# Kernel optimization log

Hardware: AMD Instinct MI355X
Metric: run time of the kernel (lower is better)

The kernel has to match this reference:

```python
import jax, jax.numpy as jnp
import numpy as np
import math

D_MODEL = 512
N_HEADS = 8
MAX_SEQ_LEN = 4096
DENSITY = 0.3


def _make_random_mask(key, seq_len, density=DENSITY):
    # rand < density, symmetrized via (m + m.T)/2, clamped to [0,1], diag = 1
    u = jax.random.uniform(key, (seq_len, seq_len), dtype=jnp.float32)
    m = (u < density).astype(jnp.float32)
    m = jnp.clip((m + m.T) * 0.5, 0.0, 1.0)
    return m.at[jnp.diag_indices(seq_len)].set(1.0)


def setup_inputs() -> dict:
    key = jax.random.key(0)
    ks = jax.random.split(key, 10)
    B, T, C = 2, 4096, D_MODEL
    scale = 1.0 / math.sqrt(C)
    x = jax.random.normal(ks[0], (B, T, C), dtype=jnp.float32)
    mask = _make_random_mask(ks[1], MAX_SEQ_LEN)[:T, :T]
    # Linear weights stored as (in, out): y = x @ W + b
    Wq = jax.random.normal(ks[2], (C, C), dtype=jnp.float32) * scale
    Wk = jax.random.normal(ks[3], (C, C), dtype=jnp.float32) * scale
    Wv = jax.random.normal(ks[4], (C, C), dtype=jnp.float32) * scale
    Wo = jax.random.normal(ks[5], (C, C), dtype=jnp.float32) * scale
    bq = jax.random.normal(ks[6], (C,), dtype=jnp.float32) * scale
    bk = jax.random.normal(ks[7], (C,), dtype=jnp.float32) * scale
    bv = jax.random.normal(ks[8], (C,), dtype=jnp.float32) * scale
    bo = jax.random.normal(ks[9], (C,), dtype=jnp.float32) * scale
    return {"x": x, "mask": mask, "Wq": Wq, "bq": bq, "Wk": Wk, "bk": bk,
            "Wv": Wv, "bv": bv, "Wo": Wo, "bo": bo}


def reference(x, mask, Wq, bq, Wk, bk, Wv, bv, Wo, bo):
    B, T, C = x.shape
    H = N_HEADS
    dk = C // H
    q = (x @ Wq + bq).reshape(B, T, H, dk)
    k = (x @ Wk + bk).reshape(B, T, H, dk)
    v = (x @ Wv + bv).reshape(B, T, H, dk)
    # scores: [B, H, T, T]
    attn = jnp.einsum('bthd,bshd->bhts', q, k) / math.sqrt(dk)
    attn = attn * mask[None, None, :, :]  # multiplicative mask PRE-softmax
    p = jax.nn.softmax(attn, axis=-1)
    out = jnp.einsum('bhts,bshd->bthd', p, v).reshape(B, T, C)
    return out @ Wo + bo
```

## Files before the change

kernel.cpp:

```cpp
#include <hip/hip_runtime.h>
#include <math.h>

#define D_MODEL 512
#define N_HEADS 8
#define DK 64
#define QSCALE (0.0625f * 1.44269504089f)

typedef __attribute__((ext_vector_type(8))) short short8;
typedef __attribute__((ext_vector_type(4))) float f32x4;
typedef __attribute__((ext_vector_type(16))) float f32x16;

typedef __attribute__((address_space(1))) const unsigned as1_uint;
typedef __attribute__((address_space(3))) unsigned as3_uint;

__device__ __forceinline__ unsigned short f2bf(float f) {
    unsigned u = __builtin_bit_cast(unsigned, f);
    u = (u + 0x7fff + ((u >> 16) & 1)) >> 16;
    return (unsigned short)u;
}

__global__ __launch_bounds__(256) void cvt_x_kernel(const float* __restrict__ x,
                                                    unsigned short* __restrict__ xb, int n8)
{
    int i = blockIdx.x * 256 + threadIdx.x;
    if (i >= n8) return;
    float4 a = ((const float4*)x)[i * 2];
    float4 b = ((const float4*)x)[i * 2 + 1];
    short8 o;
    o[0] = f2bf(a.x); o[1] = f2bf(a.y); o[2] = f2bf(a.z); o[3] = f2bf(a.w);
    o[4] = f2bf(b.x); o[5] = f2bf(b.y); o[6] = f2bf(b.z); o[7] = f2bf(b.w);
    ((short8*)xb)[i] = o;
}

__global__ __launch_bounds__(256) void cvt_mask_kernel(const float* __restrict__ m,
                                                       unsigned char* __restrict__ mu, int n4)
{
    int i = blockIdx.x * 256 + threadIdx.x;
    if (i >= n4) return;
    float4 v = ((const float4*)m)[i];
    uchar4 o = { (unsigned char)(v.x * 2.0f + 0.5f),
                 (unsigned char)(v.y * 2.0f + 0.5f),
                 (unsigned char)(v.z * 2.0f + 0.5f),
                 (unsigned char)(v.w * 2.0f + 0.5f) };
    ((uchar4*)mu)[i] = o;
}

__global__ __launch_bounds__(256) void cvt_wt4_kernel(
    const float* __restrict__ Wq, const float* __restrict__ Wk,
    const float* __restrict__ Wv, const float* __restrict__ Wo,
    unsigned short* __restrict__ Wt)
{
    __shared__ float tile[64][65];
    int z = blockIdx.z;
    const float* W = (z == 0) ? Wq : (z == 1) ? Wk : (z == 2) ? Wv : Wo;
    unsigned short* dst = Wt + (size_t)z * D_MODEL * D_MODEL;
    int t = threadIdx.x;
    int c0 = blockIdx.x * 64;
    int r0 = blockIdx.y * 64;
    #pragma unroll
    for (int i = 0; i < 16; i++) {
        int e = i * 256 + t, r = e >> 6, c = e & 63;
        tile[c][r] = W[(size_t)(r0 + r) * D_MODEL + c0 + c];
    }
    __syncthreads();
    #pragma unroll
    for (int i = 0; i < 16; i++) {
        int e = i * 256 + t, n = e >> 6, kk = e & 63;
        dst[(size_t)(c0 + n) * D_MODEL + r0 + kk] = f2bf(tile[n][kk]);
    }
}

__global__ __launch_bounds__(512) void gemm_qkv_kernel(
    const unsigned short* __restrict__ A, const unsigned short* __restrict__ Wt,
    const float* __restrict__ bq, const float* __restrict__ bk, const float* __restrict__ bv,
    unsigned short* __restrict__ qb, unsigned short* __restrict__ kb,
    unsigned short* __restrict__ vb, int M, int T)
{
    constexpr int K = D_MODEL;
    __shared__ unsigned short As[2][128 * 32];
    __shared__ unsigned short Bs[2][128 * 32];
    int t = threadIdx.x;
    int lane = t & 63, w = t >> 6;
    int ql = lane & 15, kg = lane >> 4;
    int m0 = blockIdx.y * 128, n0 = blockIdx.x * 128;
    int wm = w >> 2, wn = w & 3;
    bool vmode = (n0 >= 1024);

    const unsigned short* srcA = A + (size_t)(m0 + (t >> 2)) * K + (t & 3) * 8;
    const unsigned short* srcB = Wt + (size_t)(n0 + (t >> 2)) * K + (t & 3) * 8;

    f32x4 acc[4][2];
    #pragma unroll
    for (int i = 0; i < 4; i++)
        #pragma unroll
        for (int j = 0; j < 2; j++) { f32x4 z = {0.f, 0.f, 0.f, 0.f}; acc[i][j] = z; }

    constexpr int NIT = K / 32;
    int cur = 0;
    __builtin_amdgcn_global_load_lds((as1_uint*)(srcA),
        (as3_uint*)((char*)&As[0][0] + w * 1024), 16, 0, 0);
    __builtin_amdgcn_global_load_lds((as1_uint*)(srcB),
        (as3_uint*)((char*)&Bs[0][0] + w * 1024), 16, 0, 0);
    __syncthreads();

    for (int it = 0; it < NIT; ++it) {
        if (it + 1 < NIT) {
            int k0 = (it + 1) * 32;
            __builtin_amdgcn_global_load_lds((as1_uint*)(srcA + k0),
                (as3_uint*)((char*)&As[cur ^ 1][0] + w * 1024), 16, 0, 0);
            __builtin_amdgcn_global_load_lds((as1_uint*)(srcB + k0),
                (as3_uint*)((char*)&Bs[cur ^ 1][0] + w * 1024), 16, 0, 0);
        }
        short8 af[4], bfr[2];
        #pragma unroll
        for (int fm = 0; fm < 4; fm++)
            af[fm] = *(const short8*)((const char*)&As[cur][0] + (wm * 64 + fm * 16 + ql) * 64 + kg * 16);
        #pragma unroll
        for (int fn = 0; fn < 2; fn++)
            bfr[fn] = *(const short8*)((const char*)&Bs[cur][0] + (wn * 32 + fn * 16 + ql) * 64 + kg * 16);
        if (vmode) {
            #pragma unroll
            for (int fm = 0; fm < 4; fm++)
                #pragma unroll
                for (int fn = 0; fn < 2; fn++)
                    acc[fm][fn] = __builtin_amdgcn_mfma_f32_16x16x32_bf16(bfr[fn], af[fm], acc[fm][fn], 0, 0, 0);
        } else {
            #pragma unroll
            for (int fm = 0; fm < 4; fm++)
                #pragma unroll
                for (int fn = 0; fn < 2; fn++)
                    acc[fm][fn] = __builtin_amdgcn_mfma_f32_16x16x32_bf16(af[fm], bfr[fn], acc[fm][fn], 0, 0, 0);
        }
        __syncthreads();
        cur ^= 1;
    }

    #pragma unroll
    for (int fm = 0; fm < 4; fm++) {
        #pragma unroll
        for (int fn = 0; fn < 2; fn++) {
            if (vmode) {
                int m = m0 + wm * 64 + fm * 16 + ql;
                int b = m / T, tt = m % T;
                #pragma unroll
                for (int r = 0; r < 4; r++) {
                    int n = (n0 - 1024) + wn * 32 + fn * 16 + kg * 4 + r;
                    float val = acc[fm][fn][r] + bv[n];
                    int h = n >> 6, d = n & 63;
                    vb[((size_t)(b * N_HEADS + h) * DK + d) * T + tt] = f2bf(val);
                }
            } else {
                int n = n0 + wn * 32 + fn * 16 + ql;
                int nn = n & 511;
                bool isq = (n0 < 512);
                float bn = isq ? bq[nn] : bk[nn];
                unsigned short* dst = isq ? qb : kb;
                int h = nn >> 6, d = nn & 63;
                #pragma unroll
                for (int r = 0; r < 4; r++) {
                    int m = m0 + wm * 64 + fm * 16 + kg * 4 + r;
                    int b = m / T, tt = m % T;
                    float val = acc[fm][fn][r] + bn;
                    if (isq) val *= QSCALE;
                    dst[((size_t)(b * N_HEADS + h) * T + tt) * DK + d] = f2bf(val);
                }
            }
        }
    }
}

__global__ __launch_bounds__(512) void gemm_out_kernel(
    const unsigned short* __restrict__ A, const unsigned short* __restrict__ Bt,
    const float* __restrict__ bias, float* __restrict__ outp, int M)
{
    constexpr int K = D_MODEL;
    __shared__ unsigned short As[2][128 * 32];
    __shared__ unsigned short Bs[2][128 * 32];
    int t = threadIdx.x;
    int lane = t & 63, w = t >> 6;
    int ql = lane & 15, kg = lane >> 4;
    int m0 = blockIdx.y * 128, n0 = blockIdx.x * 128;
    int wm = w >> 2, wn = w & 3;

    const unsigned short* srcA = A + (size_t)(m0 + (t >> 2)) * K + (t & 3) * 8;
    const unsigned short* srcB = Bt + (size_t)(n0 + (t >> 2)) * K + (t & 3) * 8;

    f32x4 acc[4][2];
    #pragma unroll
    for (int i = 0; i < 4; i++)
        #pragma unroll
        for (int j = 0; j < 2; j++) { f32x4 z = {0.f, 0.f, 0.f, 0.f}; acc[i][j] = z; }

    constexpr int NIT = K / 32;
    int cur = 0;
    __builtin_amdgcn_global_load_lds((as1_uint*)(srcA),
        (as3_uint*)((char*)&As[0][0] + w * 1024), 16, 0, 0);
    __builtin_amdgcn_global_load_lds((as1_uint*)(srcB),
        (as3_uint*)((char*)&Bs[0][0] + w * 1024), 16, 0, 0);
    __syncthreads();

    for (int it = 0; it < NIT; ++it) {
        if (it + 1 < NIT) {
            int k0 = (it + 1) * 32;
            __builtin_amdgcn_global_load_lds((as1_uint*)(srcA + k0),
                (as3_uint*)((char*)&As[cur ^ 1][0] + w * 1024), 16, 0, 0);
            __builtin_amdgcn_global_load_lds((as1_uint*)(srcB + k0),
                (as3_uint*)((char*)&Bs[cur ^ 1][0] + w * 1024), 16, 0, 0);
        }
        short8 af[4], bfr[2];
        #pragma unroll
        for (int fm = 0; fm < 4; fm++)
            af[fm] = *(const short8*)((const char*)&As[cur][0] + (wm * 64 + fm * 16 + ql) * 64 + kg * 16);
        #pragma unroll
        for (int fn = 0; fn < 2; fn++)
            bfr[fn] = *(const short8*)((const char*)&Bs[cur][0] + (wn * 32 + fn * 16 + ql) * 64 + kg * 16);
        #pragma unroll
        for (int fm = 0; fm < 4; fm++)
            #pragma unroll
            for (int fn = 0; fn < 2; fn++)
                acc[fm][fn] = __builtin_amdgcn_mfma_f32_16x16x32_bf16(af[fm], bfr[fn], acc[fm][fn], 0, 0, 0);
        __syncthreads();
        cur ^= 1;
    }

    #pragma unroll
    for (int fm = 0; fm < 4; fm++) {
        #pragma unroll
        for (int fn = 0; fn < 2; fn++) {
            int n = n0 + wn * 32 + fn * 16 + ql;
            float bn = bias[n];
            #pragma unroll
            for (int r = 0; r < 4; r++) {
                int m = m0 + wm * 64 + fm * 16 + kg * 4 + r;
                outp[(size_t)m * D_MODEL + n] = acc[fm][fn][r] + bn;
            }
        }
    }
}

__global__ __launch_bounds__(256) void attn_mfma_kernel(
    const unsigned short* __restrict__ q, const unsigned short* __restrict__ k,
    const unsigned short* __restrict__ v, const unsigned char* __restrict__ mu,
    unsigned short* __restrict__ out, int B, int T)
{
    __shared__ unsigned short Ks[2][64 * 64];
    __shared__ unsigned short Vt[2][64 * 64];

    int t = threadIdx.x;
    int lane = t & 63, w = t >> 6;
    int ln = lane & 31, hi = lane >> 5;

    int n = blockIdx.x;
    int nbh = B * N_HEADS;
    int nqt = T / 128;
    int bh, qt;
    if (nbh == 16 && nqt == 32) {
        int xcd = n & 7, s = n >> 3;
        bh = xcd * 2 + (s >> 5);
        qt = s & 31;
    } else {
        bh = n / nqt;
        qt = n % nqt;
    }
    int hh = bh & (N_HEADS - 1), b = bh >> 3;
    int qr0 = qt * 128;

    const char* kbase = (const char*)(k + (size_t)bh * T * DK);
    const char* vbase = (const char*)(v + (size_t)bh * DK * T);

    int lin0 = w * 1024 + lane * 16;
    int lin1 = 4096 + lin0;
    int row0 = lin0 >> 7, row1 = lin1 >> 7;
    int sw0 = (row0 & 7) << 4, sw1 = (row1 & 7) << 4;
    const char* gK0 = kbase + (lin0 ^ sw0);
    const char* gK1 = kbase + (lin1 ^ sw1);
    const char* gV0 = vbase + (size_t)row0 * (2 * T) + ((lin0 & 127) ^ sw0);
    const char* gV1 = vbase + (size_t)row1 * (2 * T) + ((lin1 & 127) ^ sw1);

    short8 qfr[4];
    {
        const unsigned short* qrow = q + ((size_t)bh * T + qr0 + w * 32 + ln) * DK + hi * 8;
        #pragma unroll
        for (int ks = 0; ks < 4; ks++)
            qfr[ks] = *(const short8*)(qrow + ks * 16);
    }

    const unsigned char* mbase = mu + (size_t)(qr0 + w * 32 + ln) * T + 4 * hi;

    f32x16 oacc[2];
    #pragma unroll
    for (int db = 0; db < 2; db++)
        #pragma unroll
        for (int i = 0; i < 16; i++) oacc[db][i] = 0.f;
    float lacc = 0.f;

    unsigned mcur[8];
    #pragma unroll
    for (int rb = 0; rb < 2; rb++)
        #pragma unroll
        for (int g = 0; g < 4; g++)
            mcur[rb * 4 + g] = *(const unsigned*)(mbase + rb * 32 + g * 8);
    __builtin_amdgcn_global_load_lds((as1_uint*)gK0, (as3_uint*)((char*)&Ks[0][0] + lin0), 16, 0, 0);
    __builtin_amdgcn_global_load_lds((as1_uint*)gK1, (as3_uint*)((char*)&Ks[0][0] + lin1), 16, 0, 0);
    __builtin_amdgcn_global_load_lds((as1_uint*)gV0, (as3_uint*)((char*)&Vt[0][0] + lin0), 16, 0, 0);
    __builtin_amdgcn_global_load_lds((as1_uint*)gV1, (as3_uint*)((char*)&Vt[0][0] + lin1), 16, 0, 0);

    int ntiles = T / 64;
    for (int kt = 0; kt < ntiles; kt++) {
        __syncthreads();
        int cur = kt & 1;
        bool havenext = (kt + 1) < ntiles;

        unsigned mnxt[8];
        if (havenext) {
            const unsigned char* mp = mbase + (size_t)(kt + 1) * 64;
            #pragma unroll
            for (int rb = 0; rb < 2; rb++)
                #pragma unroll
                for (int g = 0; g < 4; g++)
                    mnxt[rb * 4 + g] = *(const unsigned*)(mp + rb * 32 + g * 8);
            size_t ko = (size_t)(kt + 1) * 8192;
            size_t vo = (size_t)(kt + 1) * 128;
            __builtin_amdgcn_global_load_lds((as1_uint*)(gK0 + ko),
                (as3_uint*)((char*)&Ks[cur ^ 1][0] + lin0), 16, 0, 0);
            __builtin_amdgcn_global_load_lds((as1_uint*)(gK1 + ko),
                (as3_uint*)((char*)&Ks[cur ^ 1][0] + lin1), 16, 0, 0);
            __builtin_amdgcn_global_load_lds((as1_uint*)(gV0 + vo),
                (as3_uint*)((char*)&Vt[cur ^ 1][0] + lin0), 16, 0, 0);
            __builtin_amdgcn_global_load_lds((as1_uint*)(gV1 + vo),
                (as3_uint*)((char*)&Vt[cur ^ 1][0] + lin1), 16, 0, 0);
        }

        f32x16 sacc[2];
        #pragma unroll
        for (int rb = 0; rb < 2; rb++)
            #pragma unroll
            for (int i = 0; i < 16; i++) sacc[rb][i] = 0.f;
        __builtin_amdgcn_s_setprio(1);
        #pragma unroll
        for (int ks = 0; ks < 4; ks++) {
            #pragma unroll
            for (int rb = 0; rb < 2; rb++) {
                int row = rb * 32 + ln;
                short8 kf = *(const short8*)((const char*)&Ks[cur][0] +
                            ((row * 128 + ks * 32 + hi * 16) ^ ((row & 7) << 4)));
                sacc[rb] = __builtin_amdgcn_mfma_f32_32x32x16_bf16(kf, qfr[ks], sacc[rb], 0, 0, 0);
            }
        }
        __builtin_amdgcn_s_setprio(0);

        short8 pa[4];
        #pragma unroll
        for (int rb = 0; rb < 2; rb++) {
            float p[16];
            #pragma unroll
            for (int g = 0; g < 4; g++) {
                unsigned mw = mcur[rb * 4 + g];
                float p0 = __builtin_amdgcn_exp2f(sacc[rb][g * 4 + 0] * (float)(mw & 0xffu));
                float p1 = __builtin_amdgcn_exp2f(sacc[rb][g * 4 + 1] * (float)((mw >> 8) & 0xffu));
                float p2 = __builtin_amdgcn_exp2f(sacc[rb][g * 4 + 2] * (float)((mw >> 16) & 0xffu));
                float p3 = __builtin_amdgcn_exp2f(sacc[rb][g * 4 + 3] * (float)(mw >> 24));
                p[g * 4 + 0] = p0; p[g * 4 + 1] = p1; p[g * 4 + 2] = p2; p[g * 4 + 3] = p3;
                lacc += (p0 + p1) + (p2 + p3);
            }
            #pragma unroll
            for (int kl = 0; kl < 2; kl++) {
                int b0 = kl * 8;
                unsigned d0, d1, d2, d3;
                asm("v_cvt_pk_bf16_f32 %0, %1, %2" : "=v"(d0) : "v"(p[b0 + 0]), "v"(p[b0 + 1]));
                asm("v_cvt_pk_bf16_f32 %0, %1, %2" : "=v"(d1) : "v"(p[b0 + 2]), "v"(p[b0 + 3]));
                asm("v_cvt_pk_bf16_f32 %0, %1, %2" : "=v"(d2) : "v"(p[b0 + 4]), "v"(p[b0 + 5]));
                asm("v_cvt_pk_bf16_f32 %0, %1, %2" : "=v"(d3) : "v"(p[b0 + 6]), "v"(p[b0 + 7]));
                asm("v_permlane32_swap_b32 %0, %1" : "+v"(d0), "+v"(d2));
                asm("v_permlane32_swap_b32 %0, %1" : "+v"(d1), "+v"(d3));
                uint4 fr = { d0, d1, d2, d3 };
                pa[rb * 2 + kl] = __builtin_bit_cast(short8, fr);
            }
        }

        __builtin_amdgcn_s_setprio(1);
        #pragma unroll
        for (int ks = 0; ks < 4; ks++) {
            #pragma unroll
            for (int db = 0; db < 2; db++) {
                int row = db * 32 + ln;
                short8 vb = *(const short8*)((const char*)&Vt[cur][0] +
                            ((row * 128 + ks * 32 + hi * 16) ^ ((row & 7) << 4)));
                oacc[db] = __builtin_amdgcn_mfma_f32_32x32x16_bf16(pa[ks], vb, oacc[db], 0, 0, 0);
            }
        }
        __builtin_amdgcn_s_setprio(0);

        if (havenext) {
            #pragma unroll
            for (int c = 0; c < 8; c++) mcur[c] = mnxt[c];
        }
    }

    lacc += __shfl_xor(lacc, 32, 64);

    #pragma unroll
    for (int reg = 0; reg < 16; reg++) {
        int qoff = (reg & 3) + 8 * (reg >> 2) + 4 * hi;
        float linv = 1.0f / __shfl(lacc, qoff, 64);
        size_t rowo = ((size_t)b * T + qr0 + w * 32 + qoff) * D_MODEL + hh * DK + ln;
        out[rowo]      = f2bf(oacc[0][reg] * linv);
        out[rowo + 32] = f2bf(oacc[1][reg] * linv);
    }
}

extern "C" void kernel_launch(void* const* d_in, const int* in_sizes, int n_in,
                              void* d_out, int out_size, void* d_ws, size_t ws_size,
                              hipStream_t stream) {
    const float* x    = (const float*)d_in[0];
    const float* mask = (const float*)d_in[1];
    const float* Wq   = (const float*)d_in[2];
    const float* bq   = (const float*)d_in[3];
    const float* Wk   = (const float*)d_in[4];
    const float* bk   = (const float*)d_in[5];
    const float* Wv   = (const float*)d_in[6];
    const float* bv   = (const float*)d_in[7];
    const float* Wo   = (const float*)d_in[8];
    const float* bo   = (const float*)d_in[9];

    int T = (int)(sqrt((double)in_sizes[1]) + 0.5);
    int C = D_MODEL;
    int B = in_sizes[0] / (T * C);
    int M = B * T;

    size_t MK = (size_t)M * C;
    unsigned short* xb  = (unsigned short*)d_ws;
    unsigned short* Wtq = xb + MK;
    unsigned short* Wto = Wtq + 3 * (size_t)C * C;
    unsigned short* qb  = Wtq + 4 * (size_t)C * C;
    unsigned short* kb  = qb + MK;
    unsigned short* vb  = kb + MK;
    unsigned short* attb = vb + MK;
    unsigned char*  mu  = (unsigned char*)(attb + MK);

    int n8 = (int)(MK / 8);
    cvt_x_kernel<<<(n8 + 255) / 256, 256, 0, stream>>>(x, xb, n8);
    int n4 = T * T / 4;
    cvt_mask_kernel<<<(n4 + 255) / 256, 256, 0, stream>>>(mask, mu, n4);
    dim3 wtg(C / 64, C / 64, 4);
    cvt_wt4_kernel<<<wtg, 256, 0, stream>>>(Wq, Wk, Wv, Wo, Wtq);

    dim3 gq(3 * C / 128, M / 128, 1);
    gemm_qkv_kernel<<<gq, 512, 0, stream>>>(xb, Wtq, bq, bk, bv, qb, kb, vb, M, T);

    int nblocks = (B * N_HEADS) * (T / 128);
    attn_mfma_kernel<<<nblocks, 256, 0, stream>>>(qb, kb, vb, mu, attb, B, T);

    dim3 gg(C / 128, M / 128, 1);
    gemm_out_kernel<<<gg, 512, 0, stream>>>(attb, Wto, bo, (float*)d_out, M);
}
```

Baseline: 211.4 us.

## Software-pipeline PV MFMA one tile behind QK and compute row sums via MFMA

Restructures the attention loop so the P·V MFMAs for the previous key tile run right after the current tile's QK MFMAs. The exp/convert work can then overlap with matrix-core work, and a third V buffer in LDS keeps the previous tile's V alive. The row-sum of probabilities is now accumulated by an extra MFMA against a ones vector instead of scalar adds plus shuffles. This adds one MFMA per k-step, a third LDS buffer, extra accumulator registers and a drain step after the loop, with some risk of register pressure and lower occupancy.

```diff
diff --git a/kernel.cpp b/kernel.cpp
--- a/kernel.cpp
+++ b/kernel.cpp
@@ -244,7 +244,7 @@
     unsigned short* __restrict__ out, int B, int T)
 {
     __shared__ unsigned short Ks[2][64 * 64];
-    __shared__ unsigned short Vt[2][64 * 64];
+    __shared__ unsigned short Vt[3][64 * 64];
 
     int t = threadIdx.x;
     int lane = t & 63, w = t >> 6;
@@ -285,14 +285,23 @@
             qfr[ks] = *(const short8*)(qrow + ks * 16);
     }
 
+    short8 ones;
+    #pragma unroll
+    for (int i = 0; i < 8; i++) ones[i] = (short)0x3F80;
+
     const unsigned char* mbase = mu + (size_t)(qr0 + w * 32 + ln) * T + 4 * hi;
 
-    f32x16 oacc[2];
+    f32x16 oacc[2], oacc_l;
     #pragma unroll
     for (int db = 0; db < 2; db++)
         #pragma unroll
         for (int i = 0; i < 16; i++) oacc[db][i] = 0.f;
-    float lacc = 0.f;
+    #pragma unroll
+    for (int i = 0; i < 16; i++) oacc_l[i] = 0.f;
+
+    short8 pa[4];
+    #pragma unroll
+    for (int i = 0; i < 4; i++) pa[i] = ones;
 
     unsigned mcur[8];
     #pragma unroll
@@ -306,9 +315,12 @@
     __builtin_amdgcn_global_load_lds((as1_uint*)gV1, (as3_uint*)((char*)&Vt[0][0] + lin1), 16, 0, 0);
 
     int ntiles = T / 64;
+    int vc = 0;
     for (int kt = 0; kt < ntiles; kt++) {
         __syncthreads();
-        int cur = kt & 1;
+        int kcur = kt & 1;
+        int vp = (vc + 2) % 3;
+        int vn = (vc + 1) % 3;
         bool havenext = (kt + 1) < ntiles;
 
         unsigned mnxt[8];
@@ -322,13 +334,13 @@
             size_t ko = (size_t)(kt + 1) * 8192;
             size_t vo = (size_t)(kt + 1) * 128;
             __builtin_amdgcn_global_load_lds((as1_uint*)(gK0 + ko),
-                (as3_uint*)((char*)&Ks[cur ^ 1][0] + lin0), 16, 0, 0);
+                (as3_uint*)((char*)&Ks[kcur ^ 1][0] + lin0), 16, 0, 0);
             __builtin_amdgcn_global_load_lds((as1_uint*)(gK1 + ko),
-                (as3_uint*)((char*)&Ks[cur ^ 1][0] + lin1), 16, 0, 0);
+                (as3_uint*)((char*)&Ks[kcur ^ 1][0] + lin1), 16, 0, 0);
             __builtin_amdgcn_global_load_lds((as1_uint*)(gV0 + vo),
-                (as3_uint*)((char*)&Vt[cur ^ 1][0] + lin0), 16, 0, 0);
+                (as3_uint*)((char*)&Vt[vn][0] + lin0), 16, 0, 0);
             __builtin_amdgcn_global_load_lds((as1_uint*)(gV1 + vo),
-                (as3_uint*)((char*)&Vt[cur ^ 1][0] + lin1), 16, 0, 0);
+                (as3_uint*)((char*)&Vt[vn][0] + lin1), 16, 0, 0);
         }
 
         f32x16 sacc[2];
@@ -342,14 +354,27 @@
             #pragma unroll
             for (int rb = 0; rb < 2; rb++) {
                 int row = rb * 32 + ln;
-                short8 kf = *(const short8*)((const char*)&Ks[cur][0] +
+                short8 kf = *(const short8*)((const char*)&Ks[kcur][0] +
                             ((row * 128 + ks * 32 + hi * 16) ^ ((row & 7) << 4)));
                 sacc[rb] = __builtin_amdgcn_mfma_f32_32x32x16_bf16(kf, qfr[ks], sacc[rb], 0, 0, 0);
             }
         }
+
+        if (kt > 0) {
+            #pragma unroll
+            for (int ks = 0; ks < 4; ks++) {
+                #pragma unroll
+                for (int db = 0; db < 2; db++) {
+                    int row = db * 32 + ln;
+                    short8 vb = *(const short8*)((const char*)&Vt[vp][0] +
+                                ((row * 128 + ks * 32 + hi * 16) ^ ((row & 7) << 4)));
+                    oacc[db] = __builtin_amdgcn_mfma_f32_32x32x16_bf16(pa[ks], vb, oacc[db], 0, 0, 0);
+                }
+                oacc_l = __builtin_amdgcn_mfma_f32_32x32x16_bf16(pa[ks], ones, oacc_l, 0, 0, 0);
+            }
+        }
         __builtin_amdgcn_s_setprio(0);
 
-        short8 pa[4];
         #pragma unroll
         for (int rb = 0; rb < 2; rb++) {
             float p[16];
@@ -361,7 +386,6 @@
                 float p2 = __builtin_amdgcn_exp2f(sacc[rb][g * 4 + 2] * (float)((mw >> 16) & 0xffu));
                 float p3 = __builtin_amdgcn_exp2f(sacc[rb][g * 4 + 3] * (float)(mw >> 24));
                 p[g * 4 + 0] = p0; p[g * 4 + 1] = p1; p[g * 4 + 2] = p2; p[g * 4 + 3] = p3;
-                lacc += (p0 + p1) + (p2 + p3);
             }
             #pragma unroll
             for (int kl = 0; kl < 2; kl++) {
@@ -378,31 +402,34 @@
             }
         }
 
+        if (havenext) {
+            #pragma unroll
+            for (int c = 0; c < 8; c++) mcur[c] = mnxt[c];
+        }
+        vc = vn;
+    }
+
+    {
+        int vp = (vc + 2) % 3;
         __builtin_amdgcn_s_setprio(1);
         #pragma unroll
         for (int ks = 0; ks < 4; ks++) {
             #pragma unroll
             for (int db = 0; db < 2; db++) {
                 int row = db * 32 + ln;
-                short8 vb = *(const short8*)((const char*)&Vt[cur][0] +
+                short8 vb = *(const short8*)((const char*)&Vt[vp][0] +
                             ((row * 128 + ks * 32 + hi * 16) ^ ((row & 7) << 4)));
                 oacc[db] = __builtin_amdgcn_mfma_f32_32x32x16_bf16(pa[ks], vb, oacc[db], 0, 0, 0);
             }
+            oacc_l = __builtin_amdgcn_mfma_f32_32x32x16_bf16(pa[ks], ones, oacc_l, 0, 0, 0);
         }
         __builtin_amdgcn_s_setprio(0);
-
-        if (havenext) {
-            #pragma unroll
-            for (int c = 0; c < 8; c++) mcur[c] = mnxt[c];
-        }
-    }
-
-    lacc += __shfl_xor(lacc, 32, 64);
+    }
 
     #pragma unroll
     for (int reg = 0; reg < 16; reg++) {
         int qoff = (reg & 3) + 8 * (reg >> 2) + 4 * hi;
-        float linv = 1.0f / __shfl(lacc, qoff, 64);
+        float linv = 1.0f / oacc_l[reg];
         size_t rowo = ((size_t)b * T + qr0 + w * 32 + qoff) * D_MODEL + hh * DK + ln;
         out[rowo]      = f2bf(oacc[0][reg] * linv);
         out[rowo + 32] = f2bf(oacc[1][reg] * linv);
```

Measured after the change: 208.7 us. No clear change (-1.3%).
